# Kernel tuning notes

Hardware: AMD Instinct MI355X
Metric: run time of the kernel (lower is better)

Reference implementation:

```python
import jax, jax.numpy as jnp
import numpy as np

RES = 128
SIGMA = 2
EPS = 1e-6
# 8 corner combinations of a voxel, [8, 3], static numpy constant
COMBOS = np.stack(np.meshgrid(*[[0, 1]] * 3, indexing='ij'), axis=-1).reshape(8, 3)


def _corner_idx_weights(points, res):
    """Trilinear corner indices and weights.
    points: [B, N, 3] in [0,1). Returns idx [B,N,8,3] int32, w [B,N,8].
    Matches torch code: weight for a corner = prod over dims of distance to
    the OPPOSITE corner coordinate, divided by voxel size.
    """
    pr = points * res
    lo = jnp.floor(pr)
    li = lo.astype(jnp.int32) % res           # lower index (mod res)
    ui = jnp.ceil(pr).astype(jnp.int32) % res  # upper index (mod res)
    frac = pr - lo                             # fractional offset in voxel
    c = COMBOS[None, None]                     # [1,1,8,3]
    idx = jnp.where(c == 1, ui[:, :, None, :], li[:, :, None, :])   # [B,N,8,3]
    wd = jnp.where(c == 1, frac[:, :, None, :], 1.0 - frac[:, :, None, :])
    w = jnp.prod(wd, axis=-1)                  # [B,N,8]
    return idx, w


def point_rasterization(points, features, res):
    """Scatter-add trilinear splatting. Returns [B, F, res, res, res]."""
    B, N, _ = points.shape
    F = features.shape[2]
    idx, w = _corner_idx_weights(points, res)
    vals = w[..., None] * features[:, :, None, :]          # [B,N,8,F]
    flat = (idx[..., 0] * res + idx[..., 1]) * res + idx[..., 2]  # [B,N,8]

    def scat(fl, v):  # fl [N,8], v [N,8,F]
        g = jnp.zeros((res * res * res, F), dtype=v.dtype)
        g = g.at[fl.reshape(-1)].add(v.reshape(-1, F))
        return g.T.reshape(F, res, res, res)

    return jax.vmap(scat)(flat, vals)


def grid_interpolation(field, points, res):
    """Trilinear gather. field: [B, res, res, res], points: [B,N,3] -> [B,N]."""
    idx, w = _corner_idx_weights(points, res)

    def gath(f, ix):  # f [res,res,res], ix [N,8,3]
        return f[ix[..., 0], ix[..., 1], ix[..., 2]]  # [N,8]

    vals = jax.vmap(gath)(field, idx)  # [B,N,8]
    return jnp.sum(w * vals, axis=-1)  # [B,N]


def _fft_freq_grid(res):
    f = jnp.fft.fftfreq(res, d=1.0 / res).astype(jnp.float32)  # integer frequencies
    return jnp.stack(jnp.meshgrid(f, f, f, indexing='ij'), axis=-1)  # [res,res,res,3]


def setup_inputs() -> dict:
    key = jax.random.key(0)
    k1, k2 = jax.random.split(key)
    points = jax.random.uniform(k1, (1, 250000, 3), dtype=jnp.float32) * 0.999
    normals = jax.random.normal(k2, (1, 250000, 3), dtype=jnp.float32)
    return {"points": points, "normals": normals}


def reference(points, normals):
    res = RES
    u = _fft_freq_grid(res)                                  # [X,Y,Z,3]
    u_sq = jnp.sum(u ** 2, axis=-1)                          # [X,Y,Z]
    g = jnp.exp(-2.0 * (SIGMA / res) ** 2 * u_sq)            # gaussian smoothing

    v = point_rasterization(points, normals, res)            # [B,3,X,Y,Z]
    v_tilde = jnp.fft.fftn(v, axes=(2, 3, 4)).transpose(0, 2, 3, 4, 1)  # [B,X,Y,Z,3]

    vec = jnp.sum(u[None] * v_tilde, axis=-1) / (u_sq[None] + EPS)      # [B,X,Y,Z]
    chi_tilde = g[None] * ((-1j / (2 * jnp.pi)) * vec)
    chi_prime = jnp.fft.ifftn(chi_tilde, axes=(1, 2, 3)).real            # [B,X,Y,Z]

    chi_c = grid_interpolation(chi_prime, points, res)        # [B,N]
    vecf = chi_prime - jnp.mean(chi_c, axis=-1)[:, None, None, None]
    chi_0 = vecf[:, 0, 0, 0]                                  # [B]
    chi = (0.5 / jnp.abs(chi_0))[:, None, None, None] * vecf
    return chi
```

## Files before the change

kernel.cpp:

```cpp
#include <hip/hip_runtime.h>
#include <math.h>

#define RES 128
#define RES2 (RES*RES)
#define RES3 (RES*RES*RES)
#define NROWS 16384

__device__ __forceinline__ int brev7(unsigned x){ return (int)(__brev(x) >> 25); }
__device__ __forceinline__ float freq_of(int s){ int k = brev7((unsigned)s); return (float)(k < 64 ? k : k - 128); }
__device__ __forceinline__ float2 cmul(float2 a, float2 b){
    return make_float2(a.x*b.x - a.y*b.y, a.x*b.y + a.y*b.x);
}
__device__ __forceinline__ float2 twd(float ang){ float s, c; __sincosf(ang, &s, &c); return make_float2(c, s); }

__device__ __forceinline__ void dif128(float2& r0, float2& r1, int tt){
    {
        float2 a = r0, b = r1;
        r0 = make_float2(a.x + b.x, a.y + b.y);
        float2 d = make_float2(a.x - b.x, a.y - b.y);
        r1 = cmul(d, twd(-(float)M_PI * (float)tt * (1.f/64.f)));
    }
    #pragma unroll
    for (int h = 32; h >= 1; h >>= 1){
        int bit = tt & h;
        int k = tt & (h - 1);
        float2 w = twd(-(float)M_PI * (float)k / (float)h);
        float2 o0 = make_float2(__shfl_xor(r0.x, h), __shfl_xor(r0.y, h));
        float2 o1 = make_float2(__shfl_xor(r1.x, h), __shfl_xor(r1.y, h));
        if (!bit){
            r0.x += o0.x; r0.y += o0.y;
            r1.x += o1.x; r1.y += o1.y;
        } else {
            r0 = cmul(make_float2(o0.x - r0.x, o0.y - r0.y), w);
            r1 = cmul(make_float2(o1.x - r1.x, o1.y - r1.y), w);
        }
    }
}

__device__ __forceinline__ void dit128(float2& r0, float2& r1, int tt){
    #pragma unroll
    for (int h = 1; h <= 32; h <<= 1){
        int bit = tt & h;
        int k = tt & (h - 1);
        float2 w = twd((float)M_PI * (float)k / (float)h);
        float2 o0 = make_float2(__shfl_xor(r0.x, h), __shfl_xor(r0.y, h));
        float2 o1 = make_float2(__shfl_xor(r1.x, h), __shfl_xor(r1.y, h));
        if (!bit){
            float2 t0 = cmul(o0, w), t1 = cmul(o1, w);
            r0.x += t0.x; r0.y += t0.y;
            r1.x += t1.x; r1.y += t1.y;
        } else {
            float2 t0 = cmul(r0, w), t1 = cmul(r1, w);
            r0 = make_float2(o0.x - t0.x, o0.y - t0.y);
            r1 = make_float2(o1.x - t1.x, o1.y - t1.y);
        }
    }
    {
        float2 w = twd((float)M_PI * (float)tt * (1.f/64.f));
        float2 b = cmul(r1, w);
        float2 a = r0;
        r0 = make_float2(a.x + b.x, a.y + b.y);
        r1 = make_float2(a.x - b.x, a.y - b.y);
    }
}

__global__ void hist_kernel(const float* __restrict__ pts, int* __restrict__ counts, int N){
    int i = blockIdx.x * blockDim.x + threadIdx.x;
    if (i >= N) return;
    float prx = pts[3*i] * RES, pry = pts[3*i+1] * RES;
    int lx = ((int)floorf(prx)) & 127, ly = ((int)floorf(pry)) & 127;
    atomicAdd(&counts[(lx << 7) | ly], 1);
}

__global__ __launch_bounds__(1024) void rowscan(const int* __restrict__ counts,
                                                int* __restrict__ starts,
                                                int* __restrict__ cursors){
    __shared__ int buf[2][1024];
    int t = threadIdx.x;
    int c[16];
    int base = t * 16;
    int s = 0;
    #pragma unroll
    for (int k = 0; k < 16; k++){ c[k] = counts[base + k]; s += c[k]; }
    buf[0][t] = s;
    __syncthreads();
    int cur = 0;
    for (int d = 1; d < 1024; d <<= 1){
        int v = buf[cur][t];
        if (t >= d) v += buf[cur][t - d];
        buf[cur ^ 1][t] = v;
        cur ^= 1;
        __syncthreads();
    }
    int incl = buf[cur][t];
    int run = incl - s;
    #pragma unroll
    for (int k = 0; k < 16; k++){ starts[base + k] = run; cursors[base + k] = run; run += c[k]; }
    if (t == 1023) starts[NROWS] = incl;
}

__global__ void scatter_sorted(const float* __restrict__ pts, const float* __restrict__ nrm,
                               int* __restrict__ cursors, float* __restrict__ sorted, int N){
    int i = blockIdx.x * blockDim.x + threadIdx.x;
    if (i >= N) return;
    float px = pts[3*i], py = pts[3*i+1], pz = pts[3*i+2];
    int lx = ((int)floorf(px * RES)) & 127, ly = ((int)floorf(py * RES)) & 127;
    int pos = atomicAdd(&cursors[(lx << 7) | ly], 1);
    float* q = sorted + (size_t)pos * 6;
    q[0] = px; q[1] = py; q[2] = pz;
    q[3] = nrm[3*i]; q[4] = nrm[3*i+1]; q[5] = nrm[3*i+2];
}

__global__ __launch_bounds__(192) void gather_z(const float* __restrict__ sorted,
                                                const int* __restrict__ starts,
                                                float2* __restrict__ zF){
    __shared__ float col[3][RES];
    int x = blockIdx.x >> 7, y = blockIdx.x & 127;
    int t = threadIdx.x;
    ((float*)col)[t] = 0.f;
    ((float*)col)[t + 192] = 0.f;
    __syncthreads();
    int xm = (x + 127) & 127, ym = (y + 127) & 127;
    int rowv0 = (xm<<7)|ym, rowv1 = (xm<<7)|y, rowv2 = (x<<7)|ym, rowv3 = (x<<7)|y;
    int rs0 = starts[rowv0], re0 = starts[rowv0+1];
    int rs1 = starts[rowv1], re1 = starts[rowv1+1];
    int rs2 = starts[rowv2], re2 = starts[rowv2+1];
    int rs3 = starts[rowv3], re3 = starts[rowv3+1];
    int p1 = re0 - rs0;
    int p2 = p1 + (re1 - rs1);
    int p3 = p2 + (re2 - rs2);
    int tot = p3 + (re3 - rs3);
    for (int base = 0; base < tot; base += 192){
        int k = base + t;
        if (k < tot){
            int i;
            if      (k < p1) i = rs0 + k;
            else if (k < p2) i = rs1 + (k - p1);
            else if (k < p3) i = rs2 + (k - p2);
            else             i = rs3 + (k - p3);
            const float* q = sorted + (size_t)i * 6;
            float prx = q[0]*RES, pry = q[1]*RES, prz = q[2]*RES;
            float flx = floorf(prx), fly = floorf(pry), flz = floorf(prz);
            float fx = prx - flx, fy = pry - fly, fz = prz - flz;
            int lxp = ((int)flx) & 127, lyp = ((int)fly) & 127, lz = ((int)flz) & 127;
            float wx = (lxp == x) ? (1.f - fx) : fx;
            float wy = (lyp == y) ? (1.f - fy) : fy;
            float wxy = wx * wy;
            float w0 = wxy * (1.f - fz), w1 = wxy * fz;
            int z1 = (lz + 1) & 127;
            atomicAdd(&col[0][lz], w0*q[3]); atomicAdd(&col[0][z1], w1*q[3]);
            atomicAdd(&col[1][lz], w0*q[4]); atomicAdd(&col[1][z1], w1*q[4]);
            atomicAdd(&col[2][lz], w0*q[5]); atomicAdd(&col[2][z1], w1*q[5]);
        }
    }
    __syncthreads();
    int w = t >> 6, tt = t & 63;
    float2 r0 = make_float2(col[w][tt], 0.f);
    float2 r1 = make_float2(col[w][tt + 64], 0.f);
    dif128(r0, r1, tt);
    float2* q = zF + (size_t)w * RES3 + (((size_t)x << 14) | ((size_t)y << 7));
    q[tt] = r0; q[tt + 64] = r1;
}

__global__ __launch_bounds__(1024) void mega_y(const float2* __restrict__ zF,
                                               float2* __restrict__ bufA,
                                               float2* __restrict__ bufB){
    __shared__ float2 tile[16][130];
    int t = threadIdx.x;
    int x = blockIdx.x >> 3, z0 = (blockIdx.x & 7) << 4;
    size_t base = ((size_t)x << 14) + (size_t)z0;
    int y0 = t >> 4, zz = t & 15, y1 = y0 + 64;
    size_t i0 = base + ((size_t)y0 << 7) + zz;
    size_t i1 = base + ((size_t)y1 << 7) + zz;
    int w = t >> 6, tt = t & 63;
    tile[zz][y0] = zF[RES3 + i0]; tile[zz][y1] = zF[RES3 + i1];
    __syncthreads();
    float2 A0 = tile[w][tt], A1 = tile[w][tt + 64];
    __syncthreads();
    dif128(A0, A1, tt);
    { float f0 = freq_of(tt), f1 = freq_of(tt + 64);
      A0.x *= f0; A0.y *= f0; A1.x *= f1; A1.y *= f1; }
    tile[zz][y0] = zF[2*(size_t)RES3 + i0]; tile[zz][y1] = zF[2*(size_t)RES3 + i1];
    __syncthreads();
    float2 C0 = tile[w][tt], C1 = tile[w][tt + 64];
    __syncthreads();
    dif128(C0, C1, tt);
    { float fz = freq_of(z0 + w);
      A0.x += fz*C0.x; A0.y += fz*C0.y; A1.x += fz*C1.x; A1.y += fz*C1.y; }
    tile[zz][y0] = zF[i0]; tile[zz][y1] = zF[i1];
    __syncthreads();
    float2 B0 = tile[w][tt], B1 = tile[w][tt + 64];
    __syncthreads();
    dif128(B0, B1, tt);
    tile[w][tt] = A0; tile[w][tt + 64] = A1;
    __syncthreads();
    bufA[i0] = tile[zz][y0]; bufA[i1] = tile[zz][y1];
    __syncthreads();
    tile[w][tt] = B0; tile[w][tt + 64] = B1;
    __syncthreads();
    bufB[i0] = tile[zz][y0]; bufB[i1] = tile[zz][y1];
}

__global__ __launch_bounds__(1024) void x_mega(const float2* __restrict__ bufB,
                                               float2* __restrict__ bufA){
    __shared__ float2 tA[16][130];
    __shared__ float2 tB[16][130];
    int t = threadIdx.x;
    int y = blockIdx.x >> 3, z0 = (blockIdx.x & 7) << 4;
    size_t base = ((size_t)y << 7) + (size_t)z0;
    int x0 = t >> 4, zz = t & 15;
    int x1 = x0 + 64;
    size_t g0 = base + ((size_t)x0 << 14) + zz;
    size_t g1 = base + ((size_t)x1 << 14) + zz;
    tA[zz][x0] = bufA[g0]; tA[zz][x1] = bufA[g1];
    tB[zz][x0] = bufB[g0]; tB[zz][x1] = bufB[g1];
    __syncthreads();
    int w = t >> 6, tt = t & 63;
    float2 a0 = tA[w][tt], a1 = tA[w][tt + 64];
    float2 b0 = tB[w][tt], b1 = tB[w][tt + 64];
    dif128(a0, a1, tt);
    dif128(b0, b1, tt);
    float fy = freq_of(y), fz = freq_of(z0 + w);
    float fyz = fy*fy + fz*fz;
    const float K = -2.f * (2.f/128.f) * (2.f/128.f);
    {
        float fx = freq_of(tt);
        float vx = a0.x + fx*b0.x, vy = a0.y + fx*b0.y;
        float usq = fx*fx + fyz;
        float s = __expf(K*usq) / ((usq + 1e-6f) * (2.f*(float)M_PI));
        a0 = make_float2(s*vy, -s*vx);
    }
    {
        float fx = freq_of(tt + 64);
        float vx = a1.x + fx*b1.x, vy = a1.y + fx*b1.y;
        float usq = fx*fx + fyz;
        float s = __expf(K*usq) / ((usq + 1e-6f) * (2.f*(float)M_PI));
        a1 = make_float2(s*vy, -s*vx);
    }
    dit128(a0, a1, tt);
    tA[w][tt] = a0; tA[w][tt + 64] = a1;
    __syncthreads();
    bufA[g0] = tA[zz][x0];
    bufA[g1] = tA[zz][x1];
}

__global__ __launch_bounds__(1024) void inv_y(float2* __restrict__ data){
    __shared__ float2 tile[16][130];
    int t = threadIdx.x;
    int x = blockIdx.x >> 3, z0 = (blockIdx.x & 7) << 4;
    size_t base = ((size_t)x << 14) + (size_t)z0;
    int y0 = t >> 4, zz = t & 15, y1 = y0 + 64;
    size_t i0 = base + ((size_t)y0 << 7) + zz;
    size_t i1 = base + ((size_t)y1 << 7) + zz;
    tile[zz][y0] = data[i0]; tile[zz][y1] = data[i1];
    __syncthreads();
    int w = t >> 6, tt = t & 63;
    float2 r0 = tile[w][tt], r1 = tile[w][tt + 64];
    dit128(r0, r1, tt);
    tile[w][tt] = r0; tile[w][tt + 64] = r1;
    __syncthreads();
    data[i0] = tile[zz][y0]; data[i1] = tile[zz][y1];
}

__global__ __launch_bounds__(256) void inv_z_c2r(const float2* __restrict__ in, float* __restrict__ out){
    int t = threadIdx.x; int wid = t >> 6, tt = t & 63;
    size_t line = (size_t)blockIdx.x * 4 + wid;
    const float2* p = in + line * RES;
    float2 r0 = p[tt], r1 = p[tt + 64];
    dit128(r0, r1, tt);
    const float sc = 1.f / (float)RES3;
    float* q = out + line * RES;
    q[tt] = r0.x * sc; q[tt + 64] = r1.x * sc;
}

__global__ void interp_sum(const float* __restrict__ chi, const float* __restrict__ pts,
                           float* __restrict__ sum, int N){
    int i = blockIdx.x * blockDim.x + threadIdx.x;
    float val = 0.f;
    if (i < N){
        float px = pts[3*i], py = pts[3*i+1], pz = pts[3*i+2];
        float prx = px * RES, pry = py * RES, prz = pz * RES;
        float lox = floorf(prx), loy = floorf(pry), loz = floorf(prz);
        int lix = ((int)lox) & 127, liy = ((int)loy) & 127, liz = ((int)loz) & 127;
        int uix = ((int)ceilf(prx)) & 127, uiy = ((int)ceilf(pry)) & 127, uiz = ((int)ceilf(prz)) & 127;
        float fx = prx - lox, fy = pry - loy, fz = prz - loz;
        #pragma unroll
        for (int cx = 0; cx < 2; cx++){
            int ix = cx ? uix : lix;
            float wx = cx ? fx : 1.f - fx;
            #pragma unroll
            for (int cy = 0; cy < 2; cy++){
                int iy = cy ? uiy : liy;
                float wxy = wx * (cy ? fy : 1.f - fy);
                #pragma unroll
                for (int cz = 0; cz < 2; cz++){
                    int iz = cz ? uiz : liz;
                    float w = wxy * (cz ? fz : 1.f - fz);
                    val += w * chi[(ix << 14) + (iy << 7) + iz];
                }
            }
        }
    }
    __shared__ float red[256];
    int tid = threadIdx.x;
    red[tid] = val;
    __syncthreads();
    #pragma unroll
    for (int s2 = 128; s2 > 0; s2 >>= 1){
        if (tid < s2) red[tid] += red[tid + s2];
        __syncthreads();
    }
    if (tid == 0) atomicAdd(sum, red[0]);
}

__global__ void final_scale(const float* __restrict__ chi, const float* __restrict__ sum,
                            float* __restrict__ out, float invN){
    int i = blockIdx.x * blockDim.x + threadIdx.x;
    if (i >= RES3) return;
    float mean = sum[0] * invN;
    float sc = 0.5f / fabsf(chi[0] - mean);
    out[i] = sc * (chi[i] - mean);
}

extern "C" void kernel_launch(void* const* d_in, const int* in_sizes, int n_in,
                              void* d_out, int out_size, void* d_ws, size_t ws_size,
                              hipStream_t stream) {
    const float* points  = (const float*)d_in[0];
    const float* normals = (const float*)d_in[1];
    float* out = (float*)d_out;
    char* ws = (char*)d_ws;

    size_t off = 0;
    float2* zF     = (float2*)(ws + off); off += (size_t)3*RES3*8;
    float2* bufA   = (float2*)(ws + off); off += (size_t)RES3*8;
    float2* bufB   = (float2*)(ws + off); off += (size_t)RES3*8;
    float*  chiP   = (float*) (ws + off); off += (size_t)RES3*4;
    float*  sumb   = (float*) (ws + off); off += 64;
    int*    counts = (int*)   (ws + off); off += (size_t)NROWS*4;
    int*    starts = (int*)   (ws + off); off += (size_t)(NROWS+1)*4;
    int*    cursors= (int*)   (ws + off); off += (size_t)NROWS*4;
    float*  sorted = (float*) (ws + off);

    int N = in_sizes[0] / 3;

    hipMemsetAsync(counts, 0, (size_t)NROWS*4, stream);
    hipMemsetAsync(sumb, 0, 16, stream);

    hist_kernel<<<(N + 255)/256, 256, 0, stream>>>(points, counts, N);
    rowscan<<<1, 1024, 0, stream>>>(counts, starts, cursors);
    scatter_sorted<<<(N + 255)/256, 256, 0, stream>>>(points, normals, cursors, sorted, N);
    gather_z<<<NROWS, 192, 0, stream>>>(sorted, starts, zF);

    mega_y<<<1024, 1024, 0, stream>>>(zF, bufA, bufB);
    x_mega<<<1024, 1024, 0, stream>>>(bufB, bufA);
    inv_y<<<1024, 1024, 0, stream>>>(bufA);
    inv_z_c2r<<<RES2/4, 256, 0, stream>>>(bufA, chiP);

    interp_sum<<<(N + 255)/256, 256, 0, stream>>>(chiP, points, sumb, N);
    final_scale<<<RES3/256, 256, 0, stream>>>(chiP, sumb, out, 1.0f / (float)N);
}
```

Measured before the change: 233.5 us.

## Gather four y-columns per block and precompute FFT twiddles once per kernel

gather_z now processes a strip of four adjacent y columns per block (768 threads) and reads a contiguous range of five sorted rows per x-slice. Each point is loaded once and splatted into up to two of the four columns, instead of being reread by four separate blocks. The FFT helpers now take twiddle factors precomputed once per thread, and kernels that run several transforms share them rather than calling sincos in every stage. The cost is more shared-memory atomics per block and more registers held for the twiddle values.

```diff
diff --git a/kernel.cpp b/kernel.cpp
--- a/kernel.cpp
+++ b/kernel.cpp
@@ -13,18 +13,30 @@
 }
 __device__ __forceinline__ float2 twd(float ang){ float s, c; __sincosf(ang, &s, &c); return make_float2(c, s); }
 
-__device__ __forceinline__ void dif128(float2& r0, float2& r1, int tt){
+struct TW { float2 s64; float2 w[6]; };
+__device__ __forceinline__ TW make_tw(int tt){
+    TW t;
+    t.s64 = twd(-(float)M_PI * (float)tt * (1.f/64.f));
+    #pragma unroll
+    for (int i = 0; i < 6; i++){
+        int h = 32 >> i;
+        t.w[i] = twd(-(float)M_PI * (float)(tt & (h - 1)) / (float)h);
+    }
+    return t;
+}
+
+__device__ __forceinline__ void dif128_t(float2& r0, float2& r1, int tt, const TW& tw){
     {
         float2 a = r0, b = r1;
         r0 = make_float2(a.x + b.x, a.y + b.y);
         float2 d = make_float2(a.x - b.x, a.y - b.y);
-        r1 = cmul(d, twd(-(float)M_PI * (float)tt * (1.f/64.f)));
-    }
-    #pragma unroll
-    for (int h = 32; h >= 1; h >>= 1){
+        r1 = cmul(d, tw.s64);
+    }
+    #pragma unroll
+    for (int i = 0; i < 6; i++){
+        int h = 32 >> i;
         int bit = tt & h;
-        int k = tt & (h - 1);
-        float2 w = twd(-(float)M_PI * (float)k / (float)h);
+        float2 w = tw.w[i];
         float2 o0 = make_float2(__shfl_xor(r0.x, h), __shfl_xor(r0.y, h));
         float2 o1 = make_float2(__shfl_xor(r1.x, h), __shfl_xor(r1.y, h));
         if (!bit){
@@ -37,12 +49,12 @@
     }
 }
 
-__device__ __forceinline__ void dit128(float2& r0, float2& r1, int tt){
-    #pragma unroll
-    for (int h = 1; h <= 32; h <<= 1){
+__device__ __forceinline__ void dit128_t(float2& r0, float2& r1, int tt, const TW& tw){
+    #pragma unroll
+    for (int i = 5; i >= 0; i--){
+        int h = 32 >> i;
         int bit = tt & h;
-        int k = tt & (h - 1);
-        float2 w = twd((float)M_PI * (float)k / (float)h);
+        float2 w = make_float2(tw.w[i].x, -tw.w[i].y);
         float2 o0 = make_float2(__shfl_xor(r0.x, h), __shfl_xor(r0.y, h));
         float2 o1 = make_float2(__shfl_xor(r1.x, h), __shfl_xor(r1.y, h));
         if (!bit){
@@ -56,7 +68,7 @@
         }
     }
     {
-        float2 w = twd((float)M_PI * (float)tt * (1.f/64.f));
+        float2 w = make_float2(tw.s64.x, -tw.s64.y);
         float2 b = cmul(r1, w);
         float2 a = r0;
         r0 = make_float2(a.x + b.x, a.y + b.y);
@@ -111,55 +123,72 @@
     q[3] = nrm[3*i]; q[4] = nrm[3*i+1]; q[5] = nrm[3*i+2];
 }
 
-__global__ __launch_bounds__(192) void gather_z(const float* __restrict__ sorted,
+__global__ __launch_bounds__(768) void gather_z(const float* __restrict__ sorted,
                                                 const int* __restrict__ starts,
                                                 float2* __restrict__ zF){
-    __shared__ float col[3][RES];
-    int x = blockIdx.x >> 7, y = blockIdx.x & 127;
+    __shared__ float col[3][4][RES];
+    int x  = blockIdx.x >> 5;
+    int y0 = (blockIdx.x & 31) << 2;
     int t = threadIdx.x;
     ((float*)col)[t] = 0.f;
-    ((float*)col)[t + 192] = 0.f;
-    __syncthreads();
-    int xm = (x + 127) & 127, ym = (y + 127) & 127;
-    int rowv0 = (xm<<7)|ym, rowv1 = (xm<<7)|y, rowv2 = (x<<7)|ym, rowv3 = (x<<7)|y;
-    int rs0 = starts[rowv0], re0 = starts[rowv0+1];
-    int rs1 = starts[rowv1], re1 = starts[rowv1+1];
-    int rs2 = starts[rowv2], re2 = starts[rowv2+1];
-    int rs3 = starts[rowv3], re3 = starts[rowv3+1];
-    int p1 = re0 - rs0;
-    int p2 = p1 + (re1 - rs1);
-    int p3 = p2 + (re2 - rs2);
-    int tot = p3 + (re3 - rs3);
-    for (int base = 0; base < tot; base += 192){
+    ((float*)col)[t + 768] = 0.f;
+    __syncthreads();
+    int xm = (x + 127) & 127;
+    int ybase = (y0 == 0) ? 127 : (y0 - 1);
+    int n1 = (y0 == 0) ? 1 : 5;
+    int n2 = 5 - n1;
+    int a_s[4], a_e[4];
+    { int r = (xm << 7) | ybase; a_s[0] = starts[r]; a_e[0] = starts[r + n1]; }
+    { int r = (xm << 7);         a_s[1] = starts[r]; a_e[1] = starts[r + n2]; }
+    { int r = (x  << 7) | ybase; a_s[2] = starts[r]; a_e[2] = starts[r + n1]; }
+    { int r = (x  << 7);         a_s[3] = starts[r]; a_e[3] = starts[r + n2]; }
+    int p1 = a_e[0] - a_s[0];
+    int p2 = p1 + (a_e[1] - a_s[1]);
+    int p3 = p2 + (a_e[2] - a_s[2]);
+    int tot = p3 + (a_e[3] - a_s[3]);
+    for (int base = 0; base < tot; base += 768){
         int k = base + t;
         if (k < tot){
             int i;
-            if      (k < p1) i = rs0 + k;
-            else if (k < p2) i = rs1 + (k - p1);
-            else if (k < p3) i = rs2 + (k - p2);
-            else             i = rs3 + (k - p3);
+            if      (k < p1) i = a_s[0] + k;
+            else if (k < p2) i = a_s[1] + (k - p1);
+            else if (k < p3) i = a_s[2] + (k - p2);
+            else             i = a_s[3] + (k - p3);
             const float* q = sorted + (size_t)i * 6;
             float prx = q[0]*RES, pry = q[1]*RES, prz = q[2]*RES;
             float flx = floorf(prx), fly = floorf(pry), flz = floorf(prz);
             float fx = prx - flx, fy = pry - fly, fz = prz - flz;
             int lxp = ((int)flx) & 127, lyp = ((int)fly) & 127, lz = ((int)flz) & 127;
             float wx = (lxp == x) ? (1.f - fx) : fx;
-            float wy = (lyp == y) ? (1.f - fy) : fy;
-            float wxy = wx * wy;
-            float w0 = wxy * (1.f - fz), w1 = wxy * fz;
             int z1 = (lz + 1) & 127;
-            atomicAdd(&col[0][lz], w0*q[3]); atomicAdd(&col[0][z1], w1*q[3]);
-            atomicAdd(&col[1][lz], w0*q[4]); atomicAdd(&col[1][z1], w1*q[4]);
-            atomicAdd(&col[2][lz], w0*q[5]); atomicAdd(&col[2][z1], w1*q[5]);
+            float n0 = q[3], nv1 = q[4], nv2 = q[5];
+            int jA = (lyp - y0) & 127;
+            int jB = (jA + 1) & 127;
+            if (jA < 4){
+                float wy = wx * (1.f - fy);
+                float w0 = wy * (1.f - fz), w1 = wy * fz;
+                atomicAdd(&col[0][jA][lz], w0*n0);  atomicAdd(&col[0][jA][z1], w1*n0);
+                atomicAdd(&col[1][jA][lz], w0*nv1); atomicAdd(&col[1][jA][z1], w1*nv1);
+                atomicAdd(&col[2][jA][lz], w0*nv2); atomicAdd(&col[2][jA][z1], w1*nv2);
+            }
+            if (jB < 4){
+                float wy = wx * fy;
+                float w0 = wy * (1.f - fz), w1 = wy * fz;
+                atomicAdd(&col[0][jB][lz], w0*n0);  atomicAdd(&col[0][jB][z1], w1*n0);
+                atomicAdd(&col[1][jB][lz], w0*nv1); atomicAdd(&col[1][jB][z1], w1*nv1);
+                atomicAdd(&col[2][jB][lz], w0*nv2); atomicAdd(&col[2][jB][z1], w1*nv2);
+            }
         }
     }
     __syncthreads();
     int w = t >> 6, tt = t & 63;
-    float2 r0 = make_float2(col[w][tt], 0.f);
-    float2 r1 = make_float2(col[w][tt + 64], 0.f);
-    dif128(r0, r1, tt);
-    float2* q = zF + (size_t)w * RES3 + (((size_t)x << 14) | ((size_t)y << 7));
-    q[tt] = r0; q[tt + 64] = r1;
+    int c = w >> 2, j = w & 3;
+    TW tw = make_tw(tt);
+    float2 r0 = make_float2(col[c][j][tt], 0.f);
+    float2 r1 = make_float2(col[c][j][tt + 64], 0.f);
+    dif128_t(r0, r1, tt, tw);
+    float2* qo = zF + (size_t)c * RES3 + (((size_t)x << 14) | ((size_t)(y0 + j) << 7));
+    qo[tt] = r0; qo[tt + 64] = r1;
 }
 
 __global__ __launch_bounds__(1024) void mega_y(const float2* __restrict__ zF,
@@ -173,25 +202,26 @@
     size_t i0 = base + ((size_t)y0 << 7) + zz;
     size_t i1 = base + ((size_t)y1 << 7) + zz;
     int w = t >> 6, tt = t & 63;
+    TW tw = make_tw(tt);
     tile[zz][y0] = zF[RES3 + i0]; tile[zz][y1] = zF[RES3 + i1];
     __syncthreads();
     float2 A0 = tile[w][tt], A1 = tile[w][tt + 64];
     __syncthreads();
-    dif128(A0, A1, tt);
+    dif128_t(A0, A1, tt, tw);
     { float f0 = freq_of(tt), f1 = freq_of(tt + 64);
       A0.x *= f0; A0.y *= f0; A1.x *= f1; A1.y *= f1; }
     tile[zz][y0] = zF[2*(size_t)RES3 + i0]; tile[zz][y1] = zF[2*(size_t)RES3 + i1];
     __syncthreads();
     float2 C0 = tile[w][tt], C1 = tile[w][tt + 64];
     __syncthreads();
-    dif128(C0, C1, tt);
+    dif128_t(C0, C1, tt, tw);
     { float fz = freq_of(z0 + w);
       A0.x += fz*C0.x; A0.y += fz*C0.y; A1.x += fz*C1.x; A1.y += fz*C1.y; }
     tile[zz][y0] = zF[i0]; tile[zz][y1] = zF[i1];
     __syncthreads();
     float2 B0 = tile[w][tt], B1 = tile[w][tt + 64];
     __syncthreads();
-    dif128(B0, B1, tt);
+    dif128_t(B0, B1, tt, tw);
     tile[w][tt] = A0; tile[w][tt + 64] = A1;
     __syncthreads();
     bufA[i0] = tile[zz][y0]; bufA[i1] = tile[zz][y1];
@@ -216,10 +246,11 @@
     tB[zz][x0] = bufB[g0]; tB[zz][x1] = bufB[g1];
     __syncthreads();
     int w = t >> 6, tt = t & 63;
+    TW tw = make_tw(tt);
     float2 a0 = tA[w][tt], a1 = tA[w][tt + 64];
     float2 b0 = tB[w][tt], b1 = tB[w][tt + 64];
-    dif128(a0, a1, tt);
-    dif128(b0, b1, tt);
+    dif128_t(a0, a1, tt, tw);
+    dif128_t(b0, b1, tt, tw);
     float fy = freq_of(y), fz = freq_of(z0 + w);
     float fyz = fy*fy + fz*fz;
     const float K = -2.f * (2.f/128.f) * (2.f/128.f);
@@ -237,7 +268,7 @@
         float s = __expf(K*usq) / ((usq + 1e-6f) * (2.f*(float)M_PI));
         a1 = make_float2(s*vy, -s*vx);
     }
-    dit128(a0, a1, tt);
+    dit128_t(a0, a1, tt, tw);
     tA[w][tt] = a0; tA[w][tt + 64] = a1;
     __syncthreads();
     bufA[g0] = tA[zz][x0];
@@ -255,8 +286,9 @@
     tile[zz][y0] = data[i0]; tile[zz][y1] = data[i1];
     __syncthreads();
     int w = t >> 6, tt = t & 63;
+    TW tw = make_tw(tt);
     float2 r0 = tile[w][tt], r1 = tile[w][tt + 64];
-    dit128(r0, r1, tt);
+    dit128_t(r0, r1, tt, tw);
     tile[w][tt] = r0; tile[w][tt + 64] = r1;
     __syncthreads();
     data[i0] = tile[zz][y0]; data[i1] = tile[zz][y1];
@@ -266,8 +298,9 @@
     int t = threadIdx.x; int wid = t >> 6, tt = t & 63;
     size_t line = (size_t)blockIdx.x * 4 + wid;
     const float2* p = in + line * RES;
+    TW tw = make_tw(tt);
     float2 r0 = p[tt], r1 = p[tt + 64];
-    dit128(r0, r1, tt);
+    dit128_t(r0, r1, tt, tw);
     const float sc = 1.f / (float)RES3;
     float* q = out + line * RES;
     q[tt] = r0.x * sc; q[tt + 64] = r1.x * sc;
@@ -349,7 +382,7 @@
     hist_kernel<<<(N + 255)/256, 256, 0, stream>>>(points, counts, N);
     rowscan<<<1, 1024, 0, stream>>>(counts, starts, cursors);
     scatter_sorted<<<(N + 255)/256, 256, 0, stream>>>(points, normals, cursors, sorted, N);
-    gather_z<<<NROWS, 192, 0, stream>>>(sorted, starts, zF);
+    gather_z<<<128*32, 768, 0, stream>>>(sorted, starts, zF);
 
     mega_y<<<1024, 1024, 0, stream>>>(zF, bufA, bufB);
     x_mega<<<1024, 1024, 0, stream>>>(bufB, bufA);
```

New measurement: 237.0 us. No clear change (+1.5%).
